# Kernel optimization log

Hardware: AMD Instinct MI355X
Metric: run time of the kernel (lower is better)

Reference implementation:

```python
import jax, jax.numpy as jnp
import numpy as np

V, D, NH, DH, DFF, NL = 32000, 512, 8, 64, 2048, 6
S, B = 512, 8
NEG = -1e18


def layer_norm(x, g, b, eps=1e-5):
    m = x.mean(-1, keepdims=True)
    v = ((x - m) ** 2).mean(-1, keepdims=True)
    return (x - m) / jnp.sqrt(v + eps) * g + b


def mha(q, k, v, Wq, bq, Wk, bk, Wv, bv, Wo, bo, mask):
    Bq, Q, _ = q.shape
    K = k.shape[1]
    qh = (q @ Wq + bq).reshape(Bq, Q, NH, DH).transpose(0, 2, 1, 3)
    kh = (k @ Wk + bk).reshape(Bq, K, NH, DH).transpose(0, 2, 1, 3)
    vh = (v @ Wv + bv).reshape(Bq, K, NH, DH).transpose(0, 2, 1, 3)
    scores = jnp.einsum('bhqd,bhkd->bhqk', qh, kh) / np.sqrt(DH).astype(np.float32)
    scores = jnp.where(mask[:, None, :, :], NEG, scores)
    attn = jax.nn.softmax(scores, axis=-1)
    ctx = jnp.einsum('bhqk,bhkd->bhqd', attn, vh).transpose(0, 2, 1, 3).reshape(Bq, Q, NH * DH)
    return ctx @ Wo + bo


def positional_encoding(seq_len):
    pos = jnp.arange(seq_len, dtype=jnp.float32)[:, None]
    div = jnp.exp(jnp.arange(0, D, 2, dtype=jnp.float32) * (-np.log(10000.0) / D))
    pe = jnp.zeros((seq_len, D), jnp.float32)
    pe = pe.at[:, 0::2].set(jnp.sin(pos * div))
    pe = pe.at[:, 1::2].set(jnp.cos(pos * div))
    return pe


def setup_inputs() -> dict:
    key = jax.random.key(0)
    ks = iter(jax.random.split(key, 64))
    sc = 0.02
    pn = lambda shape: jax.random.normal(next(ks), shape, jnp.float32) * sc
    inp = {}
    inp['targets'] = jax.random.randint(next(ks), (S, B), 0, V)
    inp['memory'] = jax.random.normal(next(ks), (B, S, D), jnp.float32)
    inp['trg_mask'] = jnp.broadcast_to(jnp.triu(jnp.ones((S, S), bool), 1), (B, S, S))
    inp['memory_mask'] = jnp.zeros((B, S, S), bool)
    emb = pn((V, D)).at[1].set(0.0)  # padding_idx=1
    inp['emb'] = emb
    # stacked per-layer params
    for nm in ['Wq_s', 'Wk_s', 'Wv_s', 'Wo_s', 'Wq_c', 'Wk_c', 'Wv_c', 'Wo_c']:
        inp[nm] = pn((NL, D, D))
    for nm in ['bq_s', 'bk_s', 'bv_s', 'bo_s', 'bq_c', 'bk_c', 'bv_c', 'bo_c']:
        inp[nm] = jnp.zeros((NL, D), jnp.float32)
    inp['W1'] = pn((NL, D, DFF)); inp['b1'] = jnp.zeros((NL, DFF), jnp.float32)
    inp['W2'] = pn((NL, DFF, D)); inp['b2'] = jnp.zeros((NL, D), jnp.float32)
    for nm in ['g1', 'g2', 'g3']:
        inp[nm] = jnp.ones((NL, D), jnp.float32)
    for nm in ['be1', 'be2', 'be3']:
        inp[nm] = jnp.zeros((NL, D), jnp.float32)
    return inp


def reference(targets, memory, trg_mask, memory_mask, emb,
              Wq_s, bq_s, Wk_s, bk_s, Wv_s, bv_s, Wo_s, bo_s,
              Wq_c, bq_c, Wk_c, bk_c, Wv_c, bv_c, Wo_c, bo_c,
              W1, b1, W2, b2, g1, be1, g2, be2, g3, be3):
    # targets: (S, B) ints; embedding + sqrt(d) scale + sinusoidal PE
    x = emb[targets] * np.sqrt(D).astype(np.float32)      # (S, B, D)
    x = x + positional_encoding(targets.shape[0])[:, None, :]
    x = x.transpose(1, 0, 2)                              # (B, S, D)
    for i in range(NL):
        sa = mha(x, x, x, Wq_s[i], bq_s[i], Wk_s[i], bk_s[i], Wv_s[i], bv_s[i],
                 Wo_s[i], bo_s[i], trg_mask)
        x = layer_norm(x + sa, g1[i], be1[i])
        ca = mha(x, memory, memory, Wq_c[i], bq_c[i], Wk_c[i], bk_c[i], Wv_c[i], bv_c[i],
                 Wo_c[i], bo_c[i], memory_mask)
        x = layer_norm(x + ca, g2[i], be2[i])
        ff = jax.nn.relu(x @ W1[i] + b1[i]) @ W2[i] + b2[i]
        x = layer_norm(x + ff, g3[i], be3[i])
    return x
```

## Files before the change

kernel.cpp:

```cpp
#include <hip/hip_runtime.h>

typedef unsigned short u16;
typedef unsigned int   u32;
typedef __attribute__((ext_vector_type(4))) u16   u16x4;
typedef __attribute__((ext_vector_type(8))) u16   u16x8;
typedef __attribute__((ext_vector_type(8))) __bf16 bf16x8;
typedef __attribute__((ext_vector_type(4))) float f32x4;

#define DEV static __device__ __forceinline__

constexpr int DIM = 512, NHEAD = 8, DHEAD = 64, DFFN = 2048, NLAY = 6, SEQ = 512, BATCH = 8;
constexpr int MROWS = BATCH * SEQ;
constexpr long HD = (long)SEQ * DHEAD;
constexpr long SQ = (long)DIM * DIM;

DEV float bf2f(u16 u) { union { u32 i; float f; } x; x.i = (u32)u << 16; return x.f; }
DEV u16 f2bf(float f) { union { float f; u32 i; } x; x.f = f; u32 r = x.i + 0x7fffu + ((x.i >> 16) & 1u); return (u16)(r >> 16); }

DEV void gl_lds16(const u16* g, u16* l) {
    __builtin_amdgcn_global_load_lds((const __attribute__((address_space(1))) u32*)(const void*)g,
                                     (__attribute__((address_space(3))) u32*)(void*)l, 16, 0, 0);
}

struct TP { const float* in[8]; u16* out[8]; long ls[8]; };

__global__ __launch_bounds__(256) void transpose8(TP p)
{
    __shared__ u16 t[32][33];
    int z = blockIdx.z, which = z / NLAY, l = z % NLAY;
    const float* in = p.in[which] + (long)l * SQ;
    u16* out = p.out[which] + (long)l * p.ls[which];
    int k0 = blockIdx.y * 32, n0 = blockIdx.x * 32;
    int tx = threadIdx.x & 31, ty = threadIdx.x >> 5;
    #pragma unroll
    for (int i = ty; i < 32; i += 8) t[i][tx] = f2bf(in[(long)(k0 + i) * 512 + n0 + tx]);
    __syncthreads();
    #pragma unroll
    for (int i = ty; i < 32; i += 8) out[(long)(n0 + i) * 512 + k0 + tx] = t[tx][i];
}

__global__ __launch_bounds__(256) void transpose_w12(const float* __restrict__ W1, const float* __restrict__ W2,
                                                     u16* __restrict__ w1T, u16* __restrict__ w2T)
{
    __shared__ u16 t[32][33];
    int z = blockIdx.z;
    bool isW2 = z >= NLAY;
    int l = isW2 ? z - NLAY : z;
    const float* in = (isW2 ? W2 : W1) + (long)l * DIM * DFFN;
    u16* out = (isW2 ? w2T : w1T) + (long)l * DIM * DFFN;
    int K = isW2 ? DFFN : DIM, N = isW2 ? DIM : DFFN;
    int k0 = (isW2 ? blockIdx.x : blockIdx.y) * 32;
    int n0 = (isW2 ? blockIdx.y : blockIdx.x) * 32;
    int tx = threadIdx.x & 31, ty = threadIdx.x >> 5;
    #pragma unroll
    for (int i = ty; i < 32; i += 8) t[i][tx] = f2bf(in[(long)(k0 + i) * N + n0 + tx]);
    __syncthreads();
    #pragma unroll
    for (int i = ty; i < 32; i += 8) out[(long)(n0 + i) * K + k0 + tx] = t[tx][i];
}

struct CB { const float* s[6]; };
__global__ __launch_bounds__(256) void concat2(CB p, float* __restrict__ bqkv, float* __restrict__ bqkvc)
{
    int i = blockIdx.x * 256 + threadIdx.x;
    constexpr int HALF = NLAY * 3 * DIM;
    int j = (i < HALF) ? i : i - HALF;
    int col = j & 511, wsel = (j >> 9) % 3, l = j / 1536;
    const float* s = p.s[(i < HALF ? 0 : 3) + wsel];
    (i < HALF ? bqkv : bqkvc)[j] = s[l * 512 + col];
}

__global__ __launch_bounds__(256) void prep_act(const int* __restrict__ targets, const float* __restrict__ emb,
                                                u16* __restrict__ xb,
                                                const float* __restrict__ memory, u16* __restrict__ memb)
{
    int bid = blockIdx.x;
    if (bid < 2048) {
        int t4 = (bid * 256 + threadIdx.x) * 4;
        int d = t4 & (DIM - 1);
        int s = (t4 >> 9) & (SEQ - 1);
        int b = t4 >> 18;
        int tok = targets[s * BATCH + b];
        float4 e = *(const float4*)(emb + (long)tok * DIM + d);
        u16x4 ob;
        const float ef[4] = { e.x, e.y, e.z, e.w };
        #pragma unroll
        for (int j = 0; j < 4; ++j) {
            int dd = d + j;
            float div = expf((float)(dd & ~1) * -0.017988946039016f);
            float ang = (float)s * div;
            float pe = (dd & 1) ? cosf(ang) : sinf(ang);
            ob[j] = f2bf(ef[j] * 22.627416997969522f + pe);
        }
        *(u16x4*)(xb + ((long)b * SEQ + s) * DIM + d) = ob;
    } else {
        long i = ((long)(bid - 2048) * 256 + threadIdx.x) * 4;
        float4 v = *(const float4*)(memory + i);
        u16x4 o; o.x = f2bf(v.x); o.y = f2bf(v.y); o.z = f2bf(v.z); o.w = f2bf(v.w);
        *(u16x4*)(memb + i) = o;
    }
}

DEV void scat_sd(u16* dst, int mm, int col, float v) {
    dst[(long)((mm >> 9) * NHEAD + (col >> 6)) * HD + (long)(mm & 511) * DHEAD + (col & 63)] = f2bf(v);
}
DEV void scat_ds(u16* dst, int mm, int col, float v) {
    dst[(long)((mm >> 9) * NHEAD + (col >> 6)) * HD + (long)(col & 63) * SEQ + (mm & 511)] = f2bf(v);
}

template <int BM, int BN, int BK, int EPI>
__global__ __launch_bounds__(256) void gemm_t(const u16* __restrict__ A0, const u16* __restrict__ A1,
                                              const u16* __restrict__ Bt,
                                              void* __restrict__ C0, void* __restrict__ C1, void* __restrict__ C2,
                                              const float* __restrict__ bias, int K, int ld, int ldc,
                                              int gx, int aSplit)
{
    constexpr int SLOTS = BK / 8;
    constexpr int RPC   = 512 / BK;
    constexpr int KK    = BK / 32;
    constexpr int NCHA  = BM / RPC;
    constexpr int NCH   = (BM + BN) / RPC;
    constexpr int MI    = BM / 32;
    constexpr int NI    = BN / 32;
    __shared__ __align__(16) u16 lds[2][NCH * 512];

    const int tid = threadIdx.x, lane = tid & 63, wid = tid >> 6;
    const int nwg = gridDim.x, bid = blockIdx.x;
    const int wg = (bid & 7) * (nwg >> 3) + (bid >> 3);
    const int m0 = (wg / gx) * BM, n0 = (wg % gx) * BN;
    const u16* A = (n0 < aSplit) ? A0 : A1;
    const int kBase = blockIdx.y * K;
    const int wr = (wid >> 1) * (BM / 2), wc = (wid & 1) * (BN / 2);
    const int fr = lane & 15, fq = lane >> 4;
    const int srow  = lane / SLOTS;
    const int sslot = lane % SLOTS;

    f32x4 acc[MI][NI] = {};

    auto stage = [&](int buf, int k0) {
        #pragma unroll
        for (int c = wid; c < NCH; c += 4) {
            int slot = sslot ^ ((c * RPC + srow) & (SLOTS - 1));
            long row = (c < NCHA) ? (long)(m0 + c * RPC + srow)
                                  : (long)(n0 + (c - NCHA) * RPC + srow);
            const u16* src = (c < NCHA) ? A : Bt;
            gl_lds16(src + row * ld + kBase + k0 + slot * 8, &lds[buf][c * 512]);
        }
    };

    const int nt = K / BK;
    stage(0, 0);
    __syncthreads();
    int cur = 0;
    const int swz = (fr & (SLOTS - 1)) << 4;
    for (int t = 0; t < nt; ++t) {
        if (t + 1 < nt) stage(cur ^ 1, (t + 1) * BK);
        const char* lb = (const char*)&lds[cur][0];
        bf16x8 a[MI][KK], b[NI][KK];
        #pragma unroll
        for (int mi = 0; mi < MI; ++mi)
            #pragma unroll
            for (int kk = 0; kk < KK; ++kk)
                a[mi][kk] = *(const bf16x8*)(lb + (wr + mi * 16 + fr) * (BK * 2) + ((kk * 64 + fq * 16) ^ swz));
        #pragma unroll
        for (int ni = 0; ni < NI; ++ni)
            #pragma unroll
            for (int kk = 0; kk < KK; ++kk)
                b[ni][kk] = *(const bf16x8*)(lb + (BM + wc + ni * 16 + fr) * (BK * 2) + ((kk * 64 + fq * 16) ^ swz));
        #pragma unroll
        for (int kk = 0; kk < KK; ++kk)
            #pragma unroll
            for (int mi = 0; mi < MI; ++mi)
                #pragma unroll
                for (int ni = 0; ni < NI; ++ni)
                    acc[mi][ni] = __builtin_amdgcn_mfma_f32_16x16x32_bf16(a[mi][kk], b[ni][kk], acc[mi][ni], 0, 0, 0);
        __syncthreads();
        cur ^= 1;
    }

    #pragma unroll
    for (int mi = 0; mi < MI; ++mi)
    #pragma unroll
    for (int ni = 0; ni < NI; ++ni)
    #pragma unroll
    for (int rr = 0; rr < 4; ++rr) {
        int mm = m0 + wr + mi * 16 + fq * 4 + rr;
        int nn = n0 + wc + ni * 16 + fr;
        float v = acc[mi][ni][rr];
        if (EPI != 5) v += bias[nn];
        if (EPI == 0) {
            ((u16*)C0)[(long)mm * ldc + nn] = f2bf(v);
        } else if (EPI == 1) {
            ((u16*)C0)[(long)mm * ldc + nn] = f2bf(fmaxf(v, 0.f));
        } else if (EPI == 5) {
            ((float*)C0)[(long)blockIdx.y * MROWS * ldc + (long)mm * ldc + nn] = v;
        } else {
            int which = nn >> 9, col = nn & 511;
            if (which == 0)      scat_sd((u16*)C0, mm, col, v);
            else if (which == 1) scat_sd((u16*)C1, mm, col, v);
            else                 scat_ds((u16*)C2, mm, col, v);
        }
    }
}

template <bool CAUSAL>
__global__ __launch_bounds__(256) void flash_attn(const u16* __restrict__ qh, const u16* __restrict__ kh,
                                                  const u16* __restrict__ vT, u16* __restrict__ ctx)
{
    constexpr int KVB = 128;
    __shared__ __align__(16) u16 Kl[2][KVB * 64];
    __shared__ __align__(16) u16 Vl[2][64 * KVB];
    __shared__ __align__(16) u16 Pl[4][16 * KVB];
    const int lane = threadIdx.x & 63, wid = threadIdx.x >> 6;
    const int head = blockIdx.x & 63, qt = blockIdx.x >> 6;
    const int q0 = qt * 64;
    const long hb = (long)head * HD;
    const int fr = lane & 15, fq = lane >> 4;
    const int swz = (fr & 7) << 4;

    bf16x8 qf[2];
    #pragma unroll
    for (int kf = 0; kf < 2; ++kf)
        qf[kf] = *(const bf16x8*)(qh + hb + (long)(q0 + wid * 16 + fr) * 64 + kf * 32 + fq * 8);

    const int nt = CAUSAL ? (q0 >> 7) + 1 : SEQ / KVB;

    auto stage = [&](int buf, int t) {
        const long kv0 = (long)t * KVB;
        const int kr = lane >> 3;
        const int kcol = ((lane & 7) ^ kr) * 8;
        for (int c = wid; c < 16; c += 4)
            gl_lds16(kh + hb + (kv0 + c * 8 + kr) * 64 + kcol, &Kl[buf][c * 512]);
        const int vr = lane >> 4;
        for (int c = wid; c < 16; c += 4) {
            int row = c * 4 + vr;
            int vcol = ((lane & 15) ^ (row & 7)) * 8;
            gl_lds16(vT + hb + (long)row * SEQ + kv0 + vcol, &Vl[buf][c * 512]);
        }
    };

    float m[4], l[4];
    #pragma unroll
    for (int r = 0; r < 4; ++r) { m[r] = -3.0e38f; l[r] = 0.f; }
    f32x4 ao[4] = {};

    stage(0, 0);
    __syncthreads();
    int cur = 0;
    for (int t = 0; t < nt; ++t) {
        if (t + 1 < nt) stage(cur ^ 1, t + 1);
        f32x4 as[8] = {};
        const char* kb = (const char*)&Kl[cur][0];
        __builtin_amdgcn_s_setprio(1);
        #pragma unroll
        for (int nf = 0; nf < 8; ++nf)
            #pragma unroll
            for (int kf = 0; kf < 2; ++kf) {
                bf16x8 kfr = *(const bf16x8*)(kb + (nf * 16 + fr) * 128 + ((kf * 64 + fq * 16) ^ swz));
                as[nf] = __builtin_amdgcn_mfma_f32_16x16x32_bf16(qf[kf], kfr, as[nf], 0, 0, 0);
            }
        __builtin_amdgcn_s_setprio(0);
        const int kv0 = t * KVB;
        const int qrow = q0 + wid * 16 + fq * 4;
        #pragma unroll
        for (int nf = 0; nf < 8; ++nf)
            #pragma unroll
            for (int rr = 0; rr < 4; ++rr) {
                float s = as[nf][rr] * 0.125f;
                if (CAUSAL && (kv0 + nf * 16 + fr > qrow + rr)) s = -3.0e38f;
                as[nf][rr] = s;
            }
        float mnew[4]; int need = 0;
        #pragma unroll
        for (int rr = 0; rr < 4; ++rr) {
            float mx = as[0][rr];
            #pragma unroll
            for (int nf = 1; nf < 8; ++nf) mx = fmaxf(mx, as[nf][rr]);
            #pragma unroll
            for (int o = 1; o < 16; o <<= 1) mx = fmaxf(mx, __shfl_xor(mx, o, 64));
            mnew[rr] = fmaxf(m[rr], mx);
            need |= (mx > m[rr] + 8.f) ? 1 : 0;
        }
        if (__any(need)) {
            #pragma unroll
            for (int rr = 0; rr < 4; ++rr) {
                float ps = __expf(m[rr] - mnew[rr]);
                m[rr] = mnew[rr];
                l[rr] *= ps;
                #pragma unroll
                for (int nf = 0; nf < 4; ++nf) ao[nf][rr] *= ps;
            }
        }
        float rsum[4] = {0.f, 0.f, 0.f, 0.f};
        u16* pw = &Pl[wid][0];
        #pragma unroll
        for (int nf = 0; nf < 8; ++nf)
            #pragma unroll
            for (int rr = 0; rr < 4; ++rr) {
                float p = __expf(as[nf][rr] - m[rr]);
                rsum[rr] += p;
                int row = fq * 4 + rr;
                int byte = (row * 256 + (nf * 16 + fr) * 2) ^ ((row & 7) << 4);
                *(u16*)((char*)pw + byte) = f2bf(p);
            }
        #pragma unroll
        for (int rr = 0; rr < 4; ++rr) {
            #pragma unroll
            for (int o = 1; o < 16; o <<= 1) rsum[rr] += __shfl_xor(rsum[rr], o, 64);
            l[rr] += rsum[rr];
        }
        const char* vb = (const char*)&Vl[cur][0];
        __builtin_amdgcn_s_setprio(1);
        #pragma unroll
        for (int kf = 0; kf < 4; ++kf) {
            int pbyte = (fr * 256 + kf * 64 + fq * 16) ^ swz;
            bf16x8 pa = *(const bf16x8*)((const char*)pw + pbyte);
            #pragma unroll
            for (int nf = 0; nf < 4; ++nf) {
                bf16x8 vf = *(const bf16x8*)(vb + (nf * 16 + fr) * 256 + ((kf * 64 + fq * 16) ^ swz));
                ao[nf] = __builtin_amdgcn_mfma_f32_16x16x32_bf16(pa, vf, ao[nf], 0, 0, 0);
            }
        }
        __builtin_amdgcn_s_setprio(0);
        __syncthreads();
        cur ^= 1;
    }
    const int b = head >> 3, h = head & 7;
    #pragma unroll
    for (int nf = 0; nf < 4; ++nf)
        #pragma unroll
        for (int rr = 0; rr < 4; ++rr) {
            int qq = q0 + wid * 16 + fq * 4 + rr;
            ctx[((long)(b * SEQ + qq)) * DIM + h * 64 + nf * 16 + fr] = f2bf(ao[nf][rr] / l[rr]);
        }
}

__global__ __launch_bounds__(256) void add_ln(u16* xb, const u16* __restrict__ y,
                                              const float* __restrict__ g, const float* __restrict__ be)
{
    int row = blockIdx.x * 4 + (threadIdx.x >> 6);
    int lane = threadIdx.x & 63;
    long off = (long)row * DIM + lane * 8;
    u16x8 xv = *(const u16x8*)(xb + off);
    u16x8 yv = *(const u16x8*)(y + off);
    float v[8];
    #pragma unroll
    for (int j = 0; j < 8; ++j) v[j] = bf2f(xv[j]) + bf2f(yv[j]);
    float sum = 0.f;
    #pragma unroll
    for (int j = 0; j < 8; ++j) sum += v[j];
    #pragma unroll
    for (int o = 32; o; o >>= 1) sum += __shfl_xor(sum, o, 64);
    float mean = sum * (1.0f / DIM);
    float vs = 0.f;
    #pragma unroll
    for (int j = 0; j < 8; ++j) { float d = v[j] - mean; vs += d * d; }
    #pragma unroll
    for (int o = 32; o; o >>= 1) vs += __shfl_xor(vs, o, 64);
    float rstd = rsqrtf(vs * (1.0f / DIM) + 1e-5f);
    u16x8 ob;
    #pragma unroll
    for (int j = 0; j < 8; ++j) {
        int col = lane * 8 + j;
        ob[j] = f2bf((v[j] - mean) * rstd * g[col] + be[col]);
    }
    *(u16x8*)(xb + off) = ob;
}

__global__ __launch_bounds__(256) void add_ln2(u16* xb, const float* __restrict__ yf,
                                               const float* __restrict__ bias,
                                               const float* __restrict__ g, const float* __restrict__ be,
                                               float* __restrict__ xf)
{
    int row = blockIdx.x * 4 + (threadIdx.x >> 6);
    int lane = threadIdx.x & 63;
    long off = (long)row * DIM + lane * 8;
    u16x8 xv = *(const u16x8*)(xb + off);
    float4 a0 = *(const float4*)(yf + off);
    float4 a1 = *(const float4*)(yf + off + 4);
    float4 b0 = *(const float4*)(yf + (long)MROWS * DIM + off);
    float4 b1 = *(const float4*)(yf + (long)MROWS * DIM + off + 4);
    float v[8] = { a0.x + b0.x, a0.y + b0.y, a0.z + b0.z, a0.w + b0.w,
                   a1.x + b1.x, a1.y + b1.y, a1.z + b1.z, a1.w + b1.w };
    #pragma unroll
    for (int j = 0; j < 8; ++j) v[j] += bf2f(xv[j]) + bias[lane * 8 + j];
    float sum = 0.f;
    #pragma unroll
    for (int j = 0; j < 8; ++j) sum += v[j];
    #pragma unroll
    for (int o = 32; o; o >>= 1) sum += __shfl_xor(sum, o, 64);
    float mean = sum * (1.0f / DIM);
    float vs = 0.f;
    #pragma unroll
    for (int j = 0; j < 8; ++j) { float d = v[j] - mean; vs += d * d; }
    #pragma unroll
    for (int o = 32; o; o >>= 1) vs += __shfl_xor(vs, o, 64);
    float rstd = rsqrtf(vs * (1.0f / DIM) + 1e-5f);
    float outv[8]; u16x8 ob;
    #pragma unroll
    for (int j = 0; j < 8; ++j) {
        int col = lane * 8 + j;
        float r = (v[j] - mean) * rstd * g[col] + be[col];
        outv[j] = r; ob[j] = f2bf(r);
    }
    *(u16x8*)(xb + off) = ob;
    if (xf) {
        *(float4*)(xf + off)     = *(const float4*)&outv[0];
        *(float4*)(xf + off + 4) = *(const float4*)&outv[4];
    }
}

extern "C" void kernel_launch(void* const* d_in, const int* in_sizes, int n_in,
                              void* d_out, int out_size, void* d_ws, size_t ws_size,
                              hipStream_t stream)
{
    const int*   targets = (const int*)  d_in[0];
    const float* memory  = (const float*)d_in[1];
    const float* emb     = (const float*)d_in[4];
    const float* Wg[8]; for (int i = 0; i < 8; ++i) Wg[i] = (const float*)d_in[5 + i];
    const float* bg[8]; for (int i = 0; i < 8; ++i) bg[i] = (const float*)d_in[13 + i];
    const float* W1  = (const float*)d_in[21];
    const float* b1  = (const float*)d_in[22];
    const float* W2  = (const float*)d_in[23];
    const float* b2  = (const float*)d_in[24];
    const float* g1  = (const float*)d_in[25];
    const float* g2  = (const float*)d_in[26];
    const float* g3  = (const float*)d_in[27];
    const float* be1 = (const float*)d_in[28];
    const float* be2 = (const float*)d_in[29];
    const float* be3 = (const float*)d_in[30];

    char* w = (char*)d_ws;
    auto take = [&](size_t n) -> char* { char* p = w; w += (n + 255) & ~(size_t)255; return p; };
    u16*   wqkvT = (u16*)take((size_t)NLAY * 3 * SQ * 2);
    u16*   wcatT = (u16*)take((size_t)NLAY * 3 * SQ * 2);
    u16*   woT   = (u16*)take((size_t)NLAY * SQ * 2);
    u16*   wocT  = (u16*)take((size_t)NLAY * SQ * 2);
    u16*   w1T   = (u16*)take((size_t)NLAY * DIM * DFFN * 2);
    u16*   w2T   = (u16*)take((size_t)NLAY * DIM * DFFN * 2);
    float* bqkv  = (float*)take((size_t)NLAY * 3 * DIM * 4);
    float* bqkvc = (float*)take((size_t)NLAY * 3 * DIM * 4);
    u16*   xb    = (u16*)  take((size_t)MROWS * DIM * 2);
    u16*   y     = (u16*)  take((size_t)MROWS * DIM * 2);
    float* yf    = (float*)take((size_t)2 * MROWS * DIM * 4);
    u16*   memb  = (u16*)  take((size_t)MROWS * DIM * 2);
    u16*   qh    = (u16*)  take((size_t)MROWS * DIM * 2);
    u16*   kh    = (u16*)  take((size_t)MROWS * DIM * 2);
    u16*   vT    = (u16*)  take((size_t)MROWS * DIM * 2);
    u16*   ctx   = (u16*)  take((size_t)MROWS * DIM * 2);
    u16*   h1    = (u16*)  take((size_t)MROWS * DFFN * 2);

    TP tp;
    tp.in[0] = Wg[0]; tp.out[0] = wqkvT;          tp.ls[0] = 3 * SQ;
    tp.in[1] = Wg[1]; tp.out[1] = wqkvT + SQ;     tp.ls[1] = 3 * SQ;
    tp.in[2] = Wg[2]; tp.out[2] = wqkvT + 2 * SQ; tp.ls[2] = 3 * SQ;
    tp.in[3] = Wg[3]; tp.out[3] = woT;            tp.ls[3] = SQ;
    tp.in[4] = Wg[4]; tp.out[4] = wcatT;          tp.ls[4] = 3 * SQ;
    tp.in[5] = Wg[5]; tp.out[5] = wcatT + SQ;     tp.ls[5] = 3 * SQ;
    tp.in[6] = Wg[6]; tp.out[6] = wcatT + 2 * SQ; tp.ls[6] = 3 * SQ;
    tp.in[7] = Wg[7]; tp.out[7] = wocT;           tp.ls[7] = SQ;
    transpose8<<<dim3(16, 16, 8 * NLAY), 256, 0, stream>>>(tp);
    transpose_w12<<<dim3(64, 16, 2 * NLAY), 256, 0, stream>>>(W1, W2, w1T, w2T);
    CB cb; cb.s[0] = bg[0]; cb.s[1] = bg[1]; cb.s[2] = bg[2];
    cb.s[3] = bg[4]; cb.s[4] = bg[5]; cb.s[5] = bg[6];
    concat2<<<2 * NLAY * 3 * DIM / 256, 256, 0, stream>>>(cb, bqkv, bqkvc);
    prep_act<<<4096, 256, 0, stream>>>(targets, emb, xb, memory, memb);

    const int BIG = 1 << 30;
    for (int i = 0; i < NLAY; ++i) {
        const u16 *wqkv = wqkvT + (long)i * 3 * SQ, *wcat = wcatT + (long)i * 3 * SQ;
        const u16 *wo = woT + (long)i * SQ, *woc = wocT + (long)i * SQ;
        const u16 *w1t = w1T + (long)i * DIM * DFFN, *w2t = w2T + (long)i * DIM * DFFN;
        const float *bo = bg[3] + i * DIM, *boc = bg[7] + i * DIM;

        gemm_t<128, 128, 64, 4><<<384, 256, 0, stream>>>(xb, xb, wqkv, qh, kh, vT, bqkv + i * 3 * DIM, DIM, DIM, 0, 12, BIG);
        flash_attn<true><<<BATCH * NHEAD * (SEQ / 64), 256, 0, stream>>>(qh, kh, vT, ctx);
        gemm_t<64, 64, 128, 0><<<512, 256, 0, stream>>>(ctx, ctx, wo, y, nullptr, nullptr, bo, DIM, DIM, DIM, 8, BIG);
        add_ln<<<MROWS / 4, 256, 0, stream>>>(xb, y, g1 + i * DIM, be1 + i * DIM);

        gemm_t<128, 128, 64, 4><<<384, 256, 0, stream>>>(xb, memb, wcat, qh, kh, vT, bqkvc + i * 3 * DIM, DIM, DIM, 0, 12, 512);
        flash_attn<false><<<BATCH * NHEAD * (SEQ / 64), 256, 0, stream>>>(qh, kh, vT, ctx);
        gemm_t<64, 64, 128, 0><<<512, 256, 0, stream>>>(ctx, ctx, woc, y, nullptr, nullptr, boc, DIM, DIM, DIM, 8, BIG);
        add_ln<<<MROWS / 4, 256, 0, stream>>>(xb, y, g2 + i * DIM, be2 + i * DIM);

        gemm_t<128, 128, 64, 1><<<512, 256, 0, stream>>>(xb, xb, w1t, h1, nullptr, nullptr, b1 + i * DFFN, DIM, DIM, DFFN, 16, BIG);
        gemm_t<64, 64, 128, 5><<<dim3(512, 2), 256, 0, stream>>>(h1, h1, w2t, yf, nullptr, nullptr, nullptr,
                                                                 DFFN / 2, DFFN, DIM, 8, BIG);
        add_ln2<<<MROWS / 4, 256, 0, stream>>>(xb, yf, b2 + i * DIM, g3 + i * DIM, be3 + i * DIM,
                                               (i == NLAY - 1) ? (float*)d_out : nullptr);
    }
}
```

Baseline: 813.8 us.

## Precompute cross-attention K/V projections for all layers in one batched GEMM

Cross-attention K and V depend only on the encoder memory, so they are now computed for all layers up front in a single z-batched GEMM with a new scatter epilogue. Inside the layer loop only the Q projection is run, with smaller tiles. This cuts per-layer launch and tail inefficiency and improves GPU fill, at the cost of extra workspace for per-layer K/V buffers.

```diff
diff --git a/kernel.cpp b/kernel.cpp
--- a/kernel.cpp
+++ b/kernel.cpp
@@ -13,6 +13,7 @@
 constexpr int MROWS = BATCH * SEQ;
 constexpr long HD = (long)SEQ * DHEAD;
 constexpr long SQ = (long)DIM * DIM;
+constexpr long ACT = (long)MROWS * DIM;
 
 DEV float bf2f(u16 u) { union { u32 i; float f; } x; x.i = (u32)u << 16; return x.f; }
 DEV u16 f2bf(float f) { union { float f; u32 i; } x; x.f = f; u32 r = x.i + 0x7fffu + ((x.i >> 16) & 1u); return (u16)(r >> 16); }
@@ -59,15 +60,19 @@
     for (int i = ty; i < 32; i += 8) out[(long)(n0 + i) * K + k0 + tx] = t[tx][i];
 }
 
-struct CB { const float* s[6]; };
-__global__ __launch_bounds__(256) void concat2(CB p, float* __restrict__ bqkv, float* __restrict__ bqkvc)
+struct CB { const float* s[5]; };
+__global__ __launch_bounds__(256) void concat2(CB p, float* __restrict__ bqkv, float* __restrict__ bkvc)
 {
     int i = blockIdx.x * 256 + threadIdx.x;
     constexpr int HALF = NLAY * 3 * DIM;
-    int j = (i < HALF) ? i : i - HALF;
-    int col = j & 511, wsel = (j >> 9) % 3, l = j / 1536;
-    const float* s = p.s[(i < HALF ? 0 : 3) + wsel];
-    (i < HALF ? bqkv : bqkvc)[j] = s[l * 512 + col];
+    if (i < HALF) {
+        int col = i & 511, wsel = (i >> 9) % 3, l = i / 1536;
+        bqkv[i] = p.s[wsel][l * 512 + col];
+    } else {
+        int j = i - HALF;
+        int col = j & 511, which = (j >> 9) & 1, l = j / 1024;
+        bkvc[j] = p.s[3 + which][l * 512 + col];
+    }
 }
 
 __global__ __launch_bounds__(256) void prep_act(const int* __restrict__ targets, const float* __restrict__ emb,
@@ -129,6 +134,10 @@
     const int wg = (bid & 7) * (nwg >> 3) + (bid >> 3);
     const int m0 = (wg / gx) * BM, n0 = (wg % gx) * BN;
     const u16* A = (n0 < aSplit) ? A0 : A1;
+    if (EPI == 3) {
+        Bt += (long)blockIdx.z * 2 * SQ;
+        bias += (long)blockIdx.z * 2 * DIM;
+    }
     const int kBase = blockIdx.y * K;
     const int wr = (wid >> 1) * (BM / 2), wc = (wid & 1) * (BN / 2);
     const int fr = lane & 15, fq = lane >> 4;
@@ -192,6 +201,10 @@
             ((u16*)C0)[(long)mm * ldc + nn] = f2bf(v);
         } else if (EPI == 1) {
             ((u16*)C0)[(long)mm * ldc + nn] = f2bf(fmaxf(v, 0.f));
+        } else if (EPI == 3) {
+            long zoff = (long)blockIdx.z * ACT;
+            if (nn < 512) scat_sd((u16*)C1 + zoff, mm, nn, v);
+            else          scat_ds((u16*)C2 + zoff, mm, nn - 512, v);
         } else if (EPI == 5) {
             ((float*)C0)[(long)blockIdx.y * MROWS * ldc + (long)mm * ldc + nn] = v;
         } else {
@@ -378,8 +391,8 @@
     u16x8 xv = *(const u16x8*)(xb + off);
     float4 a0 = *(const float4*)(yf + off);
     float4 a1 = *(const float4*)(yf + off + 4);
-    float4 b0 = *(const float4*)(yf + (long)MROWS * DIM + off);
-    float4 b1 = *(const float4*)(yf + (long)MROWS * DIM + off + 4);
+    float4 b0 = *(const float4*)(yf + ACT + off);
+    float4 b1 = *(const float4*)(yf + ACT + off + 4);
     float v[8] = { a0.x + b0.x, a0.y + b0.y, a0.z + b0.z, a0.w + b0.w,
                    a1.x + b1.x, a1.y + b1.y, a1.z + b1.z, a1.w + b1.w };
     #pragma unroll
@@ -433,53 +446,58 @@
     char* w = (char*)d_ws;
     auto take = [&](size_t n) -> char* { char* p = w; w += (n + 255) & ~(size_t)255; return p; };
     u16*   wqkvT = (u16*)take((size_t)NLAY * 3 * SQ * 2);
-    u16*   wcatT = (u16*)take((size_t)NLAY * 3 * SQ * 2);
+    u16*   wqcT  = (u16*)take((size_t)NLAY * SQ * 2);
+    u16*   wkvcT = (u16*)take((size_t)NLAY * 2 * SQ * 2);
     u16*   woT   = (u16*)take((size_t)NLAY * SQ * 2);
     u16*   wocT  = (u16*)take((size_t)NLAY * SQ * 2);
     u16*   w1T   = (u16*)take((size_t)NLAY * DIM * DFFN * 2);
     u16*   w2T   = (u16*)take((size_t)NLAY * DIM * DFFN * 2);
     float* bqkv  = (float*)take((size_t)NLAY * 3 * DIM * 4);
-    float* bqkvc = (float*)take((size_t)NLAY * 3 * DIM * 4);
-    u16*   xb    = (u16*)  take((size_t)MROWS * DIM * 2);
-    u16*   y     = (u16*)  take((size_t)MROWS * DIM * 2);
-    float* yf    = (float*)take((size_t)2 * MROWS * DIM * 4);
-    u16*   memb  = (u16*)  take((size_t)MROWS * DIM * 2);
-    u16*   qh    = (u16*)  take((size_t)MROWS * DIM * 2);
-    u16*   kh    = (u16*)  take((size_t)MROWS * DIM * 2);
-    u16*   vT    = (u16*)  take((size_t)MROWS * DIM * 2);
-    u16*   ctx   = (u16*)  take((size_t)MROWS * DIM * 2);
+    float* bkvc  = (float*)take((size_t)NLAY * 2 * DIM * 4);
+    u16*   xb    = (u16*)  take((size_t)ACT * 2);
+    u16*   y     = (u16*)  take((size_t)ACT * 2);
+    float* yf    = (float*)take((size_t)2 * ACT * 4);
+    u16*   memb  = (u16*)  take((size_t)ACT * 2);
+    u16*   qh    = (u16*)  take((size_t)ACT * 2);
+    u16*   kh    = (u16*)  take((size_t)ACT * 2);
+    u16*   vT    = (u16*)  take((size_t)ACT * 2);
+    u16*   ctx   = (u16*)  take((size_t)ACT * 2);
     u16*   h1    = (u16*)  take((size_t)MROWS * DFFN * 2);
+    u16*   khc   = (u16*)  take((size_t)NLAY * ACT * 2);
+    u16*   vTc   = (u16*)  take((size_t)NLAY * ACT * 2);
 
     TP tp;
     tp.in[0] = Wg[0]; tp.out[0] = wqkvT;          tp.ls[0] = 3 * SQ;
     tp.in[1] = Wg[1]; tp.out[1] = wqkvT + SQ;     tp.ls[1] = 3 * SQ;
     tp.in[2] = Wg[2]; tp.out[2] = wqkvT + 2 * SQ; tp.ls[2] = 3 * SQ;
     tp.in[3] = Wg[3]; tp.out[3] = woT;            tp.ls[3] = SQ;
-    tp.in[4] = Wg[4]; tp.out[4] = wcatT;          tp.ls[4] = 3 * SQ;
-    tp.in[5] = Wg[5]; tp.out[5] = wcatT + SQ;     tp.ls[5] = 3 * SQ;
-    tp.in[6] = Wg[6]; tp.out[6] = wcatT + 2 * SQ; tp.ls[6] = 3 * SQ;
+    tp.in[4] = Wg[4]; tp.out[4] = wqcT;           tp.ls[4] = SQ;
+    tp.in[5] = Wg[5]; tp.out[5] = wkvcT;          tp.ls[5] = 2 * SQ;
+    tp.in[6] = Wg[6]; tp.out[6] = wkvcT + SQ;     tp.ls[6] = 2 * SQ;
     tp.in[7] = Wg[7]; tp.out[7] = wocT;           tp.ls[7] = SQ;
     transpose8<<<dim3(16, 16, 8 * NLAY), 256, 0, stream>>>(tp);
     transpose_w12<<<dim3(64, 16, 2 * NLAY), 256, 0, stream>>>(W1, W2, w1T, w2T);
     CB cb; cb.s[0] = bg[0]; cb.s[1] = bg[1]; cb.s[2] = bg[2];
-    cb.s[3] = bg[4]; cb.s[4] = bg[5]; cb.s[5] = bg[6];
-    concat2<<<2 * NLAY * 3 * DIM / 256, 256, 0, stream>>>(cb, bqkv, bqkvc);
+    cb.s[3] = bg[5]; cb.s[4] = bg[6];
+    concat2<<<(NLAY * 3 * DIM + NLAY * 2 * DIM) / 256, 256, 0, stream>>>(cb, bqkv, bkvc);
     prep_act<<<4096, 256, 0, stream>>>(targets, emb, xb, memory, memb);
-
     const int BIG = 1 << 30;
+    gemm_t<128, 128, 64, 3><<<dim3(256, 1, NLAY), 256, 0, stream>>>(memb, memb, wkvcT, nullptr, khc, vTc,
+                                                                    bkvc, DIM, DIM, 0, 8, BIG);
+
     for (int i = 0; i < NLAY; ++i) {
-        const u16 *wqkv = wqkvT + (long)i * 3 * SQ, *wcat = wcatT + (long)i * 3 * SQ;
+        const u16 *wqkv = wqkvT + (long)i * 3 * SQ, *wqc = wqcT + (long)i * SQ;
         const u16 *wo = woT + (long)i * SQ, *woc = wocT + (long)i * SQ;
         const u16 *w1t = w1T + (long)i * DIM * DFFN, *w2t = w2T + (long)i * DIM * DFFN;
-        const float *bo = bg[3] + i * DIM, *boc = bg[7] + i * DIM;
+        const float *bo = bg[3] + i * DIM, *bqc = bg[4] + i * DIM, *boc = bg[7] + i * DIM;
 
         gemm_t<128, 128, 64, 4><<<384, 256, 0, stream>>>(xb, xb, wqkv, qh, kh, vT, bqkv + i * 3 * DIM, DIM, DIM, 0, 12, BIG);
         flash_attn<true><<<BATCH * NHEAD * (SEQ / 64), 256, 0, stream>>>(qh, kh, vT, ctx);
         gemm_t<64, 64, 128, 0><<<512, 256, 0, stream>>>(ctx, ctx, wo, y, nullptr, nullptr, bo, DIM, DIM, DIM, 8, BIG);
         add_ln<<<MROWS / 4, 256, 0, stream>>>(xb, y, g1 + i * DIM, be1 + i * DIM);
 
-        gemm_t<128, 128, 64, 4><<<384, 256, 0, stream>>>(xb, memb, wcat, qh, kh, vT, bqkvc + i * 3 * DIM, DIM, DIM, 0, 12, 512);
-        flash_attn<false><<<BATCH * NHEAD * (SEQ / 64), 256, 0, stream>>>(qh, kh, vT, ctx);
+        gemm_t<64, 64, 128, 4><<<512, 256, 0, stream>>>(xb, xb, wqc, qh, nullptr, nullptr, bqc, DIM, DIM, 0, 8, BIG);
+        flash_attn<false><<<BATCH * NHEAD * (SEQ / 64), 256, 0, stream>>>(qh, khc + (long)i * ACT, vTc + (long)i * ACT, ctx);
         gemm_t<64, 64, 128, 0><<<512, 256, 0, stream>>>(ctx, ctx, woc, y, nullptr, nullptr, boc, DIM, DIM, DIM, 8, BIG);
         add_ln<<<MROWS / 4, 256, 0, stream>>>(xb, y, g2 + i * DIM, be2 + i * DIM);
 
```

After: 832.9 us, median of 5. 1.02x slower.
